# Performance work log

Hardware: AMD Instinct MI355X
Metric: run time of the kernel (lower is better)

## Reference

```python
import jax, jax.numpy as jnp
import numpy as np

B, C, H, W = 64, 3, 64, 64
F = 96          # base_filters
K = 8           # n_mixtures
h, w = H // 2, W // 2
C0 = 2 * C      # channels of each checkerboard half
SECTIONS = [C0, C0, C0 * K, C0 * K, C0 * K]
SPLITS = [int(s) for s in np.cumsum(SECTIONS)[:-1]]
EPS = 1e-6


def conv2d(x, wgt, b):
    y = jax.lax.conv_general_dilated(x, wgt, (1, 1), 'SAME',
                                     dimension_numbers=('NCHW', 'OIHW', 'NCHW'))
    return y + b[None, :, None, None]


def layer_norm(x, g, b, eps=1e-5):
    # nn.LayerNorm(mid_shape): normalize over (C,H,W) per sample
    mu = jnp.mean(x, axis=(1, 2, 3), keepdims=True)
    var = jnp.var(x, axis=(1, 2, 3), keepdims=True)
    return (x - mu) / jnp.sqrt(var + eps) * g[None] + b[None]


def checker_split(z, odd=False):
    Bz, Cz, Hz, Wz = z.shape
    z = z.reshape(Bz, Cz, Hz // 2, 2, Wz // 2, 2)
    p00 = z[:, :, :, 0, :, 0]; p01 = z[:, :, :, 0, :, 1]
    p10 = z[:, :, :, 1, :, 0]; p11 = z[:, :, :, 1, :, 1]
    z0 = jnp.concatenate([p00, p11], axis=1)  # even checkerboard
    z1 = jnp.concatenate([p01, p10], axis=1)  # odd checkerboard
    if odd:
        z0, z1 = z1, z0
    return z0, z1


def checker_merge(z0, z1, odd=False):
    if odd:
        z0, z1 = z1, z0
    Cz = z0.shape[1] // 2
    p00, p11 = z0[:, :Cz], z0[:, Cz:]
    p01, p10 = z1[:, :Cz], z1[:, Cz:]
    Bz, _, hz, wz = p00.shape
    zi = jnp.stack([jnp.stack([p00, p01], axis=-1),
                    jnp.stack([p10, p11], axis=-1)], axis=-2)  # (B,C,h,w,2i,2j)
    z = zi.transpose(0, 1, 2, 4, 3, 5).reshape(Bz, Cz, 2 * hz, 2 * wz)
    return z


def gated_attn(x, qkv_w, qkv_b, proj_w, proj_b):
    Bx, Fx, hx, wx = x.shape
    xf = x.reshape(Bx, Fx, hx * wx).transpose(0, 2, 1)  # (B, L, F)
    qkv = xf @ qkv_w.T + qkv_b
    q, k, v = jnp.split(qkv, 3, axis=-1)
    scores = jnp.einsum('bqf,bkf->bqk', q, k) / jnp.sqrt(jnp.float32(Fx))
    attn = jax.nn.softmax(scores, axis=-1)
    o = jnp.einsum('bqk,bkf->bqf', attn, v)
    g = o @ proj_w.T + proj_b
    ga, gb = jnp.split(g, 2, axis=-1)
    out = xf + ga * jax.nn.sigmoid(gb)  # gated residual
    return out.transpose(0, 2, 1).reshape(Bx, Fx, hx, wx)


def conditioner(z1, conv1_w, conv1_b, gconv_w, gconv_b, ln1_g, ln1_b,
                qkv_w, qkv_b, proj_w, proj_b, ln2_g, ln2_b, conv2_w, conv2_b):
    x = conv2d(z1, conv1_w, conv1_b)
    g = conv2d(x, gconv_w, gconv_b)
    ga, gb = jnp.split(g, 2, axis=1)
    x = x + ga * jax.nn.sigmoid(gb)          # GatedConv2d
    x = layer_norm(x, ln1_g, ln1_b)
    x = gated_attn(x, qkv_w, qkv_b, proj_w, proj_b)
    x = layer_norm(x, ln2_g, ln2_b)
    return conv2d(x, conv2_w, conv2_b)


def _forward(z, log_df_dz, conv1_w, conv1_b, gconv_w, gconv_b, ln1_g, ln1_b,
             qkv_w, qkv_b, proj_w, proj_b, ln2_g, ln2_b, conv2_w, conv2_b,
             a_log_scale, a_bias):
    z0, z1 = checker_split(z)
    params = conditioner(z1, conv1_w, conv1_b, gconv_w, gconv_b, ln1_g, ln1_b,
                         qkv_w, qkv_b, proj_w, proj_b, ln2_g, ln2_b, conv2_w, conv2_b)
    a, b, logpi, mu, s = jnp.split(params, SPLITS, axis=1)
    a = jnp.tanh(a) * a_log_scale + a_bias
    Bz = z0.shape[0]
    logpi = jax.nn.log_softmax(logpi.reshape(Bz, K, C0, h, w), axis=1)
    mu = mu.reshape(Bz, K, C0, h, w)
    s = s.reshape(Bz, K, C0, h, w)
    # mixture-of-logistics CDF
    u = (z0[:, None] - mu) * jnp.exp(-s)
    x = jnp.sum(jnp.exp(logpi) * jax.nn.sigmoid(u), axis=1)
    log_pdf = jax.scipy.special.logsumexp(
        logpi - s + jax.nn.log_sigmoid(u) + jax.nn.log_sigmoid(-u), axis=1)
    log_df_dz = log_df_dz + jnp.sum(log_pdf.reshape(Bz, -1), axis=1)
    # logit transform
    x = jnp.clip(x, EPS, 1.0 - EPS)
    z0n = jnp.log(x) - jnp.log1p(-x)
    log_df_dz = log_df_dz + jnp.sum((-jnp.log(x) - jnp.log1p(-x)).reshape(Bz, -1), axis=1)
    # affine rescale
    z0n = z0n * jnp.exp(a) + b
    log_df_dz = log_df_dz + jnp.sum(a.reshape(Bz, -1), axis=1)
    return checker_merge(z0n, z1), log_df_dz


def setup_inputs() -> dict:
    key = jax.random.key(0)
    ks = jax.random.split(key, 10)
    sc = 0.05
    return dict(
        z=jax.random.normal(ks[0], (B, C, H, W), jnp.float32),
        log_df_dz=jnp.zeros((B,), jnp.float32),
        conv1_w=sc * jax.random.normal(ks[1], (F, C0, 3, 3), jnp.float32),
        conv1_b=jnp.zeros((F,), jnp.float32),
        gconv_w=sc * jax.random.normal(ks[2], (2 * F, F, 3, 3), jnp.float32),
        gconv_b=jnp.zeros((2 * F,), jnp.float32),
        ln1_g=jnp.ones((F, h, w), jnp.float32),
        ln1_b=jnp.zeros((F, h, w), jnp.float32),
        qkv_w=sc * jax.random.normal(ks[3], (3 * F, F), jnp.float32),
        qkv_b=jnp.zeros((3 * F,), jnp.float32),
        proj_w=sc * jax.random.normal(ks[4], (2 * F, F), jnp.float32),
        proj_b=jnp.zeros((2 * F,), jnp.float32),
        ln2_g=jnp.ones((F, h, w), jnp.float32),
        ln2_b=jnp.zeros((F, h, w), jnp.float32),
        conv2_w=sc * jax.random.normal(ks[5], (sum(SECTIONS), F, 3, 3), jnp.float32),
        conv2_b=jnp.zeros((sum(SECTIONS),), jnp.float32),
        a_log_scale=0.01 * jax.random.normal(ks[6], (1,), jnp.float32),
        a_bias=0.01 * jax.random.normal(ks[7], (1,), jnp.float32),
    )


def reference(z, log_df_dz, conv1_w, conv1_b, gconv_w, gconv_b, ln1_g, ln1_b,
              qkv_w, qkv_b, proj_w, proj_b, ln2_g, ln2_b, conv2_w, conv2_b,
              a_log_scale, a_bias):
    return _forward(z, log_df_dz, conv1_w, conv1_b, gconv_w, gconv_b, ln1_g, ln1_b,
                    qkv_w, qkv_b, proj_w, proj_b, ln2_g, ln2_b, conv2_w, conv2_b,
                    a_log_scale, a_bias)
```

## Files before the change

kernel.cpp:

```cpp
#include <hip/hip_runtime.h>
#include <cstdint>
#include <cstddef>


typedef unsigned short u16;
typedef __attribute__((ext_vector_type(8))) short short8;
typedef __attribute__((ext_vector_type(4))) float f32x4;
typedef __attribute__((ext_vector_type(16))) float f32x16;

__device__ __forceinline__ float sigm(float x){ return 1.0f/(1.0f+__expf(-x)); }

__device__ __forceinline__ u16 f2bf(float f){
    unsigned int u = __float_as_uint(f);
    u += 0x7fffu + ((u >> 16) & 1u);
    return (u16)(u >> 16);
}
__device__ __forceinline__ float bf2f(u16 v){
    unsigned int u = ((unsigned int)v) << 16;
    return __uint_as_float(u);
}

__global__ __launch_bounds__(256) void k_prep(
    const float* __restrict__ z, const float* __restrict__ c1w, const float* __restrict__ c1b,
    const float* __restrict__ gw, const float* __restrict__ c2w,
    const float* __restrict__ qkvw, const float* __restrict__ pw,
    const float* __restrict__ ln1g, const float* __restrict__ ln1b,
    const float* __restrict__ ln2g, const float* __restrict__ ln2b,
    const float* __restrict__ logdf,
    u16* __restrict__ x1b,
    u16* __restrict__ Wg, u16* __restrict__ W2,
    u16* __restrict__ Wqkv, u16* __restrict__ Wproj,
    float* __restrict__ gt1, float* __restrict__ bt1,
    float* __restrict__ gt2, float* __restrict__ bt2,
    float* __restrict__ outlog)
{
    int blk = blockIdx.x;
    int tid = threadIdx.x;
    __shared__ float tin[6][6][34];
    __shared__ __align__(16) u16 Wc[96][72];
    __shared__ __align__(16) u16 imc[128][72];

    if (blk < 512){
        int b  = blk >> 3;
        int pg = blk & 7;
        int r0 = pg*4;
        for (int e = tid; e < 96*72; e += 256){
            int oc = e/72, k = e%72;
            Wc[oc][k] = (k < 54) ? f2bf(c1w[oc*54 + k]) : (u16)0;
        }
        for (int idx = tid; idx < 6*6*34; idx += 256){
            int c = idx/204, rem = idx%204;
            int rr = rem/34, q = rem%34;
            int ii = r0 - 1 + rr, jj = q - 1;
            float v = 0.f;
            if ((unsigned)ii < 32u && (unsigned)jj < 32u){
                if (c < 3) v = z[((b*3+c)*64 + 2*ii)*64 + (2*jj+1)];
                else       v = z[((b*3+(c-3))*64 + (2*ii+1))*64 + 2*jj];
            }
            tin[c][rr][q] = v;
        }
        __syncthreads();
        for (int e = tid; e < 128*72; e += 256){
            int px = e/72, k = e%72;
            float v = 0.f;
            if (k < 54){
                int c = k/9, rr = (k%9)/3, dcc = k%3;
                v = tin[c][(px>>5)+rr][(px&31)+dcc];
            }
            imc[px][k] = f2bf(v);
        }
        __syncthreads();

        int w = tid >> 6, lane = tid & 63;
        int cc = lane & 15, gg = lane >> 4;
        f32x4 acc[2][6];
        #pragma unroll
        for (int u=0;u<2;++u)
            #pragma unroll
            for (int t=0;t<6;++t) acc[u][t] = (f32x4){0.f,0.f,0.f,0.f};

        #pragma unroll
        for (int ks=0; ks<2; ++ks){
            short8 a0 = *reinterpret_cast<const short8*>(&imc[w*32 + cc     ][ks*32 + 8*gg]);
            short8 a1 = *reinterpret_cast<const short8*>(&imc[w*32 + 16 + cc][ks*32 + 8*gg]);
            #pragma unroll
            for (int t=0; t<6; ++t){
                short8 bb = *reinterpret_cast<const short8*>(&Wc[t*16+cc][ks*32 + 8*gg]);
                acc[0][t] = __builtin_amdgcn_mfma_f32_16x16x32_bf16(a0, bb, acc[0][t], 0,0,0);
                acc[1][t] = __builtin_amdgcn_mfma_f32_16x16x32_bf16(a1, bb, acc[1][t], 0,0,0);
            }
        }

        #pragma unroll
        for (int u=0;u<2;++u){
            int p0 = pg*128 + w*32 + u*16 + gg*4;
            #pragma unroll
            for (int t=0;t<6;++t){
                int oc = t*16+cc;
                float bv = c1b[oc];
                #pragma unroll
                for (int r=0;r<4;++r)
                    x1b[((size_t)(b*1024) + p0 + r)*96 + oc] = f2bf(acc[u][t][r] + bv);
            }
        }
    } else if (blk < 1160){
        int idx = (blk-512)*256 + tid;
        int tap = idx / (192*96);
        int rem = idx - tap*192*96;
        int ocp = rem / 96, ic = rem % 96;
        int obk = ocp/96, r = ocp%96, isB = r/48, i = r%48;
        int oc = obk*48 + i + isB*96;
        Wg[idx] = f2bf(gw[(size_t)(oc*96+ic)*9 + tap]);
    } else if (blk < 1700){
        int idx = (blk-1160)*256 + tid;
        int tap = idx / (160*96);
        int rem = idx - tap*160*96;
        int oc = rem / 96, ic = rem % 96;
        W2[idx] = (oc < 156) ? f2bf(c2w[(size_t)(oc*96+ic)*9 + tap]) : (u16)0;
    } else if (blk < 1808){
        int idx = (blk-1700)*256 + tid;
        Wqkv[idx] = f2bf(qkvw[idx]);
    } else if (blk < 1880){
        int idx = (blk-1808)*256 + tid;
        int ocp = idx / 96, ic = idx % 96;
        int obk = ocp/96, r = ocp%96, isB = r/48, i = r%48;
        int oc = obk*48 + i + isB*96;
        Wproj[idx] = f2bf(pw[(size_t)oc*96 + ic]);
    } else if (blk < 2264){
        int idx = (blk-1880)*256 + tid;
        int c = idx >> 10, p = idx & 1023;
        gt1[p*96 + c] = ln1g[idx];
    } else if (blk < 2648){
        int idx = (blk-2264)*256 + tid;
        int c = idx >> 10, p = idx & 1023;
        bt1[p*96 + c] = ln1b[idx];
    } else if (blk < 3032){
        int idx = (blk-2648)*256 + tid;
        int c = idx >> 10, p = idx & 1023;
        gt2[p*96 + c] = ln2g[idx];
    } else if (blk < 3416){
        int idx = (blk-3032)*256 + tid;
        int c = idx >> 10, p = idx & 1023;
        bt2[p*96 + c] = ln2b[idx];
    } else {
        if (tid < 64) outlog[tid] = logdf[tid];
    }
}

__global__ __launch_bounds__(256,4) void k_gconv(const u16* __restrict__ Xpb,
    const u16* __restrict__ Wt, const float* __restrict__ bias,
    u16* __restrict__ outb, float* __restrict__ partials)
{
    int blk  = blockIdx.x;
    int obk  = blk & 1;
    int pblk = (blk >> 1) & 7;
    int b    = blk >> 4;
    int tid  = threadIdx.x;
    int w = tid >> 6, lane = tid & 63;
    int cc = lane & 15, gg = lane >> 4;

    __shared__ __align__(16) u16 Ws[96][104];
    __shared__ float red[8];

    f32x4 acc[2][6];
    #pragma unroll
    for (int u=0;u<2;++u)
        #pragma unroll
        for (int t=0;t<6;++t) acc[u][t] = (f32x4){0.f,0.f,0.f,0.f};

    int base = pblk*128 + w*32;
    int ia = base >> 5;
    const u16* xb = Xpb + (size_t)b*1024*96;
    const u16* wbase = Wt + (size_t)obk*96*96;

    short8 wreg[5];
    #pragma unroll
    for (int i=0;i<5;++i){
        int c = tid + 256*i;
        if (c < 1152){
            int oc=c/12, ico=(c%12)*8;
            wreg[i] = *reinterpret_cast<const short8*>(wbase + oc*96 + ico);
        }
    }

    for (int tap=0; tap<9; ++tap){
        int dr = tap/3 - 1, dc = tap%3 - 1;
        __syncthreads();
        #pragma unroll
        for (int i=0;i<5;++i){
            int c = tid + 256*i;
            if (c < 1152){
                int oc=c/12, ico=(c%12)*8;
                *reinterpret_cast<short8*>(&Ws[oc][ico]) = wreg[i];
            }
        }
        if (tap < 8){
            const u16* wn = wbase + (size_t)(tap+1)*192*96;
            #pragma unroll
            for (int i=0;i<5;++i){
                int c = tid + 256*i;
                if (c < 1152){
                    int oc=c/12, ico=(c%12)*8;
                    wreg[i] = *reinterpret_cast<const short8*>(wn + oc*96 + ico);
                }
            }
        }
        __syncthreads();

        int ii = ia + dr;
        int jj0 = cc + dc, jj1 = cc + 16 + dc;
        bool rv = ((unsigned)ii < 32u);
        bool v0 = rv && ((unsigned)jj0 < 32u);
        bool v1 = rv && ((unsigned)jj1 < 32u);
        const u16* ar0 = xb + (ptrdiff_t)(ii*32 + jj0)*96 + 8*gg;
        const u16* ar1 = xb + (ptrdiff_t)(ii*32 + jj1)*96 + 8*gg;

        #pragma unroll
        for (int ks=0; ks<3; ++ks){
            short8 a0 = {0,0,0,0,0,0,0,0};
            short8 a1 = {0,0,0,0,0,0,0,0};
            if (v0) a0 = *reinterpret_cast<const short8*>(ar0 + ks*32);
            if (v1) a1 = *reinterpret_cast<const short8*>(ar1 + ks*32);
            #pragma unroll
            for (int t=0; t<6; ++t){
                short8 bb = *reinterpret_cast<const short8*>(&Ws[t*16+cc][ks*32+8*gg]);
                acc[0][t] = __builtin_amdgcn_mfma_f32_16x16x32_bf16(a0, bb, acc[0][t], 0,0,0);
                acc[1][t] = __builtin_amdgcn_mfma_f32_16x16x32_bf16(a1, bb, acc[1][t], 0,0,0);
            }
        }
    }

    float s = 0.f, ssq = 0.f;
    #pragma unroll
    for (int u=0;u<2;++u){
        int p0 = base + u*16 + gg*4;
        #pragma unroll
        for (int t=0;t<3;++t){
            int ocA = obk*48 + t*16+cc;
            float ba = bias[ocA], bbv = bias[ocA+96];
            #pragma unroll
            for (int r=0;r<4;++r){
                float res = bf2f(Xpb[((size_t)b*1024 + p0+r)*96 + ocA]);
                float va = acc[u][t][r]   + ba;
                float vb = acc[u][t+3][r] + bbv;
                float v = res + va*sigm(vb);
                outb[((size_t)b*1024 + p0+r)*96 + ocA] = f2bf(v);
                s += v; ssq += v*v;
            }
        }
    }
    #pragma unroll
    for (int o=32;o>0;o>>=1){ s += __shfl_down(s,o,64); ssq += __shfl_down(ssq,o,64); }
    if (lane==0){ red[w]=s; red[4+w]=ssq; }
    __syncthreads();
    if (tid==0){
        int slot = b*16 + pblk*2 + obk;
        partials[slot*2+0] = red[0]+red[1]+red[2]+red[3];
        partials[slot*2+1] = red[4]+red[5]+red[6]+red[7];
    }
}

__global__ __launch_bounds__(256) void k_lne(const u16* __restrict__ xb,
    const float* __restrict__ gt, const float* __restrict__ bt,
    const float* __restrict__ partials, u16* __restrict__ out)
{
    int b = blockIdx.x / 48, rem = blockIdx.x % 48;
    float s=0.f, ss=0.f;
    #pragma unroll
    for (int i=0;i<16;++i){ s += partials[(b*16+i)*2]; ss += partials[(b*16+i)*2+1]; }
    float mu = s/98304.f;
    float r = rsqrtf(ss/98304.f - mu*mu + 1e-5f);

    int e8 = rem*256 + threadIdx.x;
    size_t base = (size_t)b*98304 + (size_t)e8*8;
    short8 x8 = *reinterpret_cast<const short8*>(xb + base);
    const float* gp = gt + e8*8;
    const float* bp = bt + e8*8;
    short8 o8;
    #pragma unroll
    for (int i=0;i<8;++i)
        o8[i] = (short)f2bf((bf2f((u16)x8[i]) - mu)*r*gp[i] + bp[i]);
    *reinterpret_cast<short8*>(out + base) = o8;
}

__global__ __launch_bounds__(256,4) void k_conv2m(const u16* __restrict__ Xpb,
    const u16* __restrict__ Wt, const float* __restrict__ bias,
    u16* __restrict__ out)
{
    int blk  = blockIdx.x;
    int obk  = blk & 1;
    int pblk = (blk >> 1) & 7;
    int b    = blk >> 4;
    int tid  = threadIdx.x;
    int w = tid >> 6, lane = tid & 63;
    int cc = lane & 15, gg = lane >> 4;

    __shared__ __align__(16) u16 Ws[80][104];

    f32x4 acc[2][5];
    #pragma unroll
    for (int u=0;u<2;++u)
        #pragma unroll
        for (int t=0;t<5;++t) acc[u][t] = (f32x4){0.f,0.f,0.f,0.f};

    int base = pblk*128 + w*32;
    int ia = base >> 5;
    const u16* xb = Xpb + (size_t)b*1024*96;
    const u16* wbase = Wt + (size_t)obk*80*96;

    short8 wreg[4];
    #pragma unroll
    for (int i=0;i<4;++i){
        int c = tid + 256*i;
        if (c < 960){
            int oc=c/12, ico=(c%12)*8;
            wreg[i] = *reinterpret_cast<const short8*>(wbase + oc*96 + ico);
        }
    }

    for (int tap=0; tap<9; ++tap){
        int dr = tap/3 - 1, dc = tap%3 - 1;
        __syncthreads();
        #pragma unroll
        for (int i=0;i<4;++i){
            int c = tid + 256*i;
            if (c < 960){
                int oc=c/12, ico=(c%12)*8;
                *reinterpret_cast<short8*>(&Ws[oc][ico]) = wreg[i];
            }
        }
        if (tap < 8){
            const u16* wn = wbase + (size_t)(tap+1)*160*96;
            #pragma unroll
            for (int i=0;i<4;++i){
                int c = tid + 256*i;
                if (c < 960){
                    int oc=c/12, ico=(c%12)*8;
                    wreg[i] = *reinterpret_cast<const short8*>(wn + oc*96 + ico);
                }
            }
        }
        __syncthreads();

        int ii = ia + dr;
        int jj0 = cc + dc, jj1 = cc + 16 + dc;
        bool rv = ((unsigned)ii < 32u);
        bool v0 = rv && ((unsigned)jj0 < 32u);
        bool v1 = rv && ((unsigned)jj1 < 32u);
        const u16* ar0 = xb + (ptrdiff_t)(ii*32 + jj0)*96 + 8*gg;
        const u16* ar1 = xb + (ptrdiff_t)(ii*32 + jj1)*96 + 8*gg;

        #pragma unroll
        for (int ks=0; ks<3; ++ks){
            short8 a0 = {0,0,0,0,0,0,0,0};
            short8 a1 = {0,0,0,0,0,0,0,0};
            if (v0) a0 = *reinterpret_cast<const short8*>(ar0 + ks*32);
            if (v1) a1 = *reinterpret_cast<const short8*>(ar1 + ks*32);
            #pragma unroll
            for (int t=0; t<5; ++t){
                short8 bb = *reinterpret_cast<const short8*>(&Ws[t*16+cc][ks*32+8*gg]);
                acc[0][t] = __builtin_amdgcn_mfma_f32_16x16x32_bf16(a0, bb, acc[0][t], 0,0,0);
                acc[1][t] = __builtin_amdgcn_mfma_f32_16x16x32_bf16(a1, bb, acc[1][t], 0,0,0);
            }
        }
    }

    #pragma unroll
    for (int u=0;u<2;++u){
        int p0 = base + u*16 + gg*4;
        #pragma unroll
        for (int t=0;t<5;++t){
            int oc = obk*80 + t*16+cc;
            if (oc < 156){
                float bv = bias[oc];
                u16* op = out + ((size_t)b*156 + oc)*1024 + p0;
                #pragma unroll
                for (int r=0;r<4;++r) op[r] = f2bf(acc[u][t][r] + bv);
            }
        }
    }
}

__global__ __launch_bounds__(256,4) void k_qkvm(const u16* __restrict__ Xpb,
    const u16* __restrict__ Wt, const float* __restrict__ bias,
    u16* __restrict__ Qb, u16* __restrict__ Kf, u16* __restrict__ Vf)
{
    int blk  = blockIdx.x;
    int obk  = blk & 1;
    int pblk = (blk >> 1) & 7;
    int b    = blk >> 4;
    int tid  = threadIdx.x;
    int w = tid >> 6, lane = tid & 63;
    int cc = lane & 15, gg = lane >> 4;
    const float scale = 0.10206207262f;

    __shared__ __align__(16) u16 Ws[144][104];
    {
        const u16* wp = Wt + (size_t)obk*144*96;
        for (int c = tid; c < 144*12; c += 256){
            int oc = c/12, ico = (c%12)*8;
            *reinterpret_cast<short8*>(&Ws[oc][ico]) =
                *reinterpret_cast<const short8*>(wp + oc*96 + ico);
        }
    }

    f32x4 acc[2][9];
    #pragma unroll
    for (int u=0;u<2;++u)
        #pragma unroll
        for (int t=0;t<9;++t) acc[u][t] = (f32x4){0.f,0.f,0.f,0.f};

    int base = pblk*128 + w*32;
    const u16* xb = Xpb + ((size_t)b*1024 + base)*96;
    __syncthreads();

    #pragma unroll
    for (int ks=0; ks<3; ++ks){
        short8 a0 = *reinterpret_cast<const short8*>(xb + (size_t)cc*96      + ks*32 + 8*gg);
        short8 a1 = *reinterpret_cast<const short8*>(xb + (size_t)(cc+16)*96 + ks*32 + 8*gg);
        #pragma unroll
        for (int t=0; t<9; ++t){
            short8 bb = *reinterpret_cast<const short8*>(&Ws[t*16+cc][ks*32+8*gg]);
            acc[0][t] = __builtin_amdgcn_mfma_f32_16x16x32_bf16(a0, bb, acc[0][t], 0,0,0);
            acc[1][t] = __builtin_amdgcn_mfma_f32_16x16x32_bf16(a1, bb, acc[1][t], 0,0,0);
        }
    }

    #pragma unroll
    for (int u=0;u<2;++u){
        int p0 = base + u*16 + gg*4;
        #pragma unroll
        for (int t=0;t<9;++t){
            int n = obk*144 + t*16+cc;
            float bv = bias[n];
            #pragma unroll
            for (int r=0;r<4;++r){
                int p = p0 + r;
                float av = acc[u][t][r] + bv;
                if (n < 96){
                    Qb[((size_t)(b*1024+p))*96 + n] = f2bf(av*scale);
                } else if (n < 192){
                    int f = n-96;
                    int jt = p>>6, kl = p&63;
                    int tt = kl>>5;
                    int lanep = (kl&31) + 32*((f>>3)&1);
                    int ks = f>>4, j = f&7;
                    Kf[(size_t)(b*16+jt)*6144 + (size_t)(((tt*6+ks)*64 + lanep))*8 + j] = f2bf(av);
                } else {
                    int f = n-192;
                    int jt = p>>6, kl = p&63;
                    int ks2 = kl>>4, hi = (kl>>3)&1, j = kl&7;
                    int ft2 = f>>5;
                    int lanep = (f&31) + 32*hi;
                    Vf[(size_t)(b*16+jt)*6144 + (size_t)(((ft2*4+ks2)*64 + lanep))*8 + j] = f2bf(av);
                }
            }
        }
    }
}

__global__ __launch_bounds__(128,2) void k_attn(const u16* __restrict__ Qb,
    const u16* __restrict__ Kf, const u16* __restrict__ Vf, u16* __restrict__ Ob)
{
    int qt = blockIdx.x >> 6;
    int b  = blockIdx.x & 63;
    int tid = threadIdx.x;
    int w  = tid >> 6;
    int lane = tid & 63;
    int ln32 = lane & 31;
    int hl = lane >> 5;

    __shared__ __align__(16) u16 Ks[6144];
    __shared__ __align__(16) u16 Vs[6144];
    __shared__ __align__(16) u16 Ps[2][2112];

    int q0 = qt*64 + w*32;

    short8 qf[6];
    {
        const u16* qrow = Qb + ((size_t)(b*1024 + q0 + ln32))*96 + hl*8;
        #pragma unroll
        for (int ks=0; ks<6; ++ks)
            qf[ks] = *reinterpret_cast<const short8*>(qrow + ks*16);
    }

    f32x16 Oacc[3];
    #pragma unroll
    for (int ft=0; ft<3; ++ft)
        #pragma unroll
        for (int r=0; r<16; ++r) Oacc[ft][r] = 0.f;
    float l_acc[16];
    #pragma unroll
    for (int r=0; r<16; ++r) l_acc[r] = 0.f;

    const u16* Kb0 = Kf + (size_t)(b*16)*6144;
    const u16* Vb0 = Vf + (size_t)(b*16)*6144;

    short8 kreg[6], vreg[6];
    #pragma unroll
    for (int i=0;i<6;++i){
        int s8 = (tid + 128*i)*8;
        kreg[i] = *reinterpret_cast<const short8*>(Kb0 + s8);
        vreg[i] = *reinterpret_cast<const short8*>(Vb0 + s8);
    }

    for (int jt=0; jt<16; ++jt){
        __syncthreads();
        #pragma unroll
        for (int i=0;i<6;++i){
            int s8 = (tid + 128*i)*8;
            *reinterpret_cast<short8*>(Ks + s8) = kreg[i];
            *reinterpret_cast<short8*>(Vs + s8) = vreg[i];
        }
        if (jt < 15){
            const u16* kn = Kb0 + (size_t)(jt+1)*6144;
            const u16* vn = Vb0 + (size_t)(jt+1)*6144;
            #pragma unroll
            for (int i=0;i<6;++i){
                int s8 = (tid + 128*i)*8;
                kreg[i] = *reinterpret_cast<const short8*>(kn + s8);
                vreg[i] = *reinterpret_cast<const short8*>(vn + s8);
            }
        }
        __syncthreads();

        f32x16 Sacc[2];
        #pragma unroll
        for (int t=0;t<2;++t)
            #pragma unroll
            for (int r=0;r<16;++r) Sacc[t][r] = 0.f;
        #pragma unroll
        for (int ks=0; ks<6; ++ks){
            #pragma unroll
            for (int t=0; t<2; ++t){
                short8 bb = *reinterpret_cast<const short8*>(Ks + ((t*6+ks)*64 + lane)*8);
                Sacc[t] = __builtin_amdgcn_mfma_f32_32x32x16_bf16(qf[ks], bb, Sacc[t], 0,0,0);
            }
        }

        #pragma unroll
        for (int t=0; t<2; ++t){
            int off0 = (t*2 + (ln32>>4))*528 + ((ln32>>3)&1)*264 + (lane&7);
            #pragma unroll
            for (int r=0; r<16; ++r){
                int q = 4*hl + (r&3) + 8*(r>>2);
                float p = __expf(Sacc[t][r]);
                l_acc[r] += p;
                Ps[w][off0 + q*8] = f2bf(p);
            }
        }

        #pragma unroll
        for (int ks2=0; ks2<4; ++ks2){
            short8 pa = *reinterpret_cast<const short8*>(&Ps[w][ks2*528 + hl*264 + ln32*8]);
            #pragma unroll
            for (int ft=0; ft<3; ++ft){
                short8 vb = *reinterpret_cast<const short8*>(Vs + ((ft*4+ks2)*64 + lane)*8);
                Oacc[ft] = __builtin_amdgcn_mfma_f32_32x32x16_bf16(pa, vb, Oacc[ft], 0,0,0);
            }
        }
    }

    #pragma unroll
    for (int r=0; r<16; ++r){
        #pragma unroll
        for (int msk=1; msk<32; msk<<=1)
            l_acc[r] += __shfl_xor(l_acc[r], msk, 64);
    }
    #pragma unroll
    for (int r=0; r<16; ++r){
        int q = 4*hl + (r&3) + 8*(r>>2);
        float linv = 1.0f / l_acc[r];
        #pragma unroll
        for (int ft=0; ft<3; ++ft)
            Ob[((size_t)(b*1024 + q0 + q))*96 + ft*32 + ln32] = f2bf(Oacc[ft][r]*linv);
    }
}

__global__ __launch_bounds__(256,4) void k_projm(const u16* __restrict__ Opb,
    const u16* __restrict__ Wt, const float* __restrict__ bias,
    const u16* __restrict__ xlnb, u16* __restrict__ outb, float* __restrict__ partials)
{
    int blk  = blockIdx.x;
    int obk  = blk & 1;
    int pblk = (blk >> 1) & 7;
    int b    = blk >> 4;
    int tid  = threadIdx.x;
    int w = tid >> 6, lane = tid & 63;
    int cc = lane & 15, gg = lane >> 4;

    __shared__ __align__(16) u16 Ws[96][104];
    __shared__ float red[8];
    {
        const u16* wp = Wt + (size_t)obk*96*96;
        for (int c = tid; c < 96*12; c += 256){
            int oc = c/12, ico = (c%12)*8;
            *reinterpret_cast<short8*>(&Ws[oc][ico]) =
                *reinterpret_cast<const short8*>(wp + oc*96 + ico);
        }
    }

    f32x4 acc[2][6];
    #pragma unroll
    for (int u=0;u<2;++u)
        #pragma unroll
        for (int t=0;t<6;++t) acc[u][t] = (f32x4){0.f,0.f,0.f,0.f};

    int base = pblk*128 + w*32;
    const u16* xb = Opb + ((size_t)b*1024 + base)*96;
    __syncthreads();

    #pragma unroll
    for (int ks=0; ks<3; ++ks){
        short8 a0 = *reinterpret_cast<const short8*>(xb + (size_t)cc*96      + ks*32 + 8*gg);
        short8 a1 = *reinterpret_cast<const short8*>(xb + (size_t)(cc+16)*96 + ks*32 + 8*gg);
        #pragma unroll
        for (int t=0; t<6; ++t){
            short8 bb = *reinterpret_cast<const short8*>(&Ws[t*16+cc][ks*32+8*gg]);
            acc[0][t] = __builtin_amdgcn_mfma_f32_16x16x32_bf16(a0, bb, acc[0][t], 0,0,0);
            acc[1][t] = __builtin_amdgcn_mfma_f32_16x16x32_bf16(a1, bb, acc[1][t], 0,0,0);
        }
    }

    const u16* resb = xlnb + (size_t)b*1024*96;
    float s = 0.f, ssq = 0.f;
    #pragma unroll
    for (int u=0;u<2;++u){
        int p0 = base + u*16 + gg*4;
        #pragma unroll
        for (int t=0;t<3;++t){
            int ocA = obk*48 + t*16+cc;
            float ba = bias[ocA], bbv = bias[ocA+96];
            #pragma unroll
            for (int r=0;r<4;++r){
                float ga = acc[u][t][r]   + ba;
                float gb = acc[u][t+3][r] + bbv;
                float res = bf2f(resb[(size_t)(p0+r)*96 + ocA]);
                float v = res + ga * sigm(gb);
                outb[((size_t)b*1024 + p0+r)*96 + ocA] = f2bf(v);
                s += v; ssq += v*v;
            }
        }
    }
    #pragma unroll
    for (int o=32;o>0;o>>=1){ s += __shfl_down(s,o,64); ssq += __shfl_down(ssq,o,64); }
    if (lane==0){ red[w]=s; red[4+w]=ssq; }
    __syncthreads();
    if (tid==0){
        int slot = b*16 + pblk*2 + obk;
        partials[slot*2+0] = red[0]+red[1]+red[2]+red[3];
        partials[slot*2+1] = red[4]+red[5]+red[6]+red[7];
    }
}

__global__ __launch_bounds__(256) void k_mix(const float* __restrict__ z,
    const u16* __restrict__ params, const float* __restrict__ a_ls_p,
    const float* __restrict__ a_b_p, float* __restrict__ out_z, float* __restrict__ out_log)
{
    int b = blockIdx.x / 24;
    int rem = blockIdx.x % 24;
    int c0 = rem / 4;
    int pix = (rem & 3)*256 + threadIdx.x;
    int i = pix >> 5, j = pix & 31;
    float als = a_ls_p[0], abv = a_b_p[0];
    const u16* pb = params + (size_t)b*156*1024;
    float logacc = 0.f;

    if (c0 < 3){
        int idx01 = ((b*3+c0)*64 + 2*i)*64 + 2*j+1;
        int idx10 = ((b*3+c0)*64 + 2*i+1)*64 + 2*j;
        out_z[idx01] = z[idx01];
        out_z[idx10] = z[idx10];
    }

    {
        float z0v = (c0<3) ? z[((b*3+c0)*64 + 2*i)*64 + 2*j]
                           : z[((b*3+(c0-3))*64 + 2*i+1)*64 + 2*j+1];
        float a_raw = bf2f(pb[(c0)*1024 + pix]);
        float bco   = bf2f(pb[(6+c0)*1024 + pix]);
        float lp[8], mu[8], sv[8];
        float m1 = -1e30f;
        #pragma unroll
        for (int k=0;k<8;++k){
            lp[k] = bf2f(pb[(12 + k*6 + c0)*1024 + pix]);
            mu[k] = bf2f(pb[(60 + k*6 + c0)*1024 + pix]);
            sv[k] = bf2f(pb[(108 + k*6 + c0)*1024 + pix]);
            m1 = fmaxf(m1, lp[k]);
        }
        float se = 0.f;
        #pragma unroll
        for (int k=0;k<8;++k) se += __expf(lp[k]-m1);
        float lse = m1 + __logf(se);
        float xm = 0.f, mt = -1e30f;
        float t[8];
        #pragma unroll
        for (int k=0;k<8;++k){
            float lpn = lp[k] - lse;
            float u = (z0v - mu[k]) * __expf(-sv[k]);
            float au = fabsf(u);
            xm += __expf(lpn) * (1.f/(1.f+__expf(-u)));
            float lss = -(au + 2.f*log1pf(__expf(-au)));
            float tk = lpn - sv[k] + lss;
            t[k] = tk; mt = fmaxf(mt, tk);
        }
        float se2 = 0.f;
        #pragma unroll
        for (int k=0;k<8;++k) se2 += __expf(t[k]-mt);
        logacc += mt + __logf(se2);
        xm = fminf(fmaxf(xm, 1e-6f), 1.f-1e-6f);
        float lx = __logf(xm), l1x = log1pf(-xm);
        logacc += -lx - l1x;
        float aa = tanhf(a_raw)*als + abv;
        float z0n = (lx - l1x)*__expf(aa) + bco;
        logacc += aa;
        int oidx = (c0<3) ? ((b*3+c0)*64 + 2*i)*64 + 2*j
                          : ((b*3+(c0-3))*64 + 2*i+1)*64 + 2*j+1;
        out_z[oidx] = z0n;
    }

    #pragma unroll
    for (int o=32;o>0;o>>=1) logacc += __shfl_down(logacc, o, 64);
    __shared__ float part[4];
    if ((threadIdx.x&63)==0) part[threadIdx.x>>6] = logacc;
    __syncthreads();
    if (threadIdx.x==0){
        atomicAdd(out_log + b, part[0]+part[1]+part[2]+part[3]);
    }
}

extern "C" void kernel_launch(void* const* d_in, const int* in_sizes, int n_in,
                              void* d_out, int out_size, void* d_ws, size_t ws_size,
                              hipStream_t stream)
{
    const float* z     = (const float*)d_in[0];
    const float* logdf = (const float*)d_in[1];
    const float* c1w   = (const float*)d_in[2];
    const float* c1b   = (const float*)d_in[3];
    const float* gw    = (const float*)d_in[4];
    const float* gcb   = (const float*)d_in[5];
    const float* ln1g  = (const float*)d_in[6];
    const float* ln1b  = (const float*)d_in[7];
    const float* qkvw  = (const float*)d_in[8];
    const float* qkvb  = (const float*)d_in[9];
    const float* pw    = (const float*)d_in[10];
    const float* pbb   = (const float*)d_in[11];
    const float* ln2g  = (const float*)d_in[12];
    const float* ln2b  = (const float*)d_in[13];
    const float* c2w   = (const float*)d_in[14];
    const float* c2b   = (const float*)d_in[15];
    const float* als   = (const float*)d_in[16];
    const float* ab    = (const float*)d_in[17];

    float* out_z   = (float*)d_out;
    float* out_log = out_z + 786432;

    float* ws     = (float*)d_ws;
    u16*   x1b    = (u16*)(ws + 0);
    u16*   xg_b   = (u16*)(ws + 3145728);
    u16*   xlnb   = (u16*)(ws + 6291456);
    u16*   Vf     = (u16*)(ws + 9437184);
    u16*   Ob     = (u16*)(ws + 12582912);
    u16*   x2b    = (u16*)(ws + 15728640);
    u16*   Qb     = x1b;
    u16*   Kf     = xg_b;
    u16*   xln2b  = xlnb;
    u16*   params = (u16*)(ws + 9437184);
    const size_t T = 19660800;
    float* gt1    = ws + T;
    float* bt1    = ws + T + 98304;
    float* gt2    = ws + T + 196608;
    float* bt2    = ws + T + 294912;
    float* part1  = ws + T + 393216;
    float* part2  = ws + T + 395264;
    u16*   Wg     = (u16*)(ws + T + 397568);
    u16*   W2     = (u16*)(ws + T + 480512);
    u16*   Wqkv   = (u16*)(ws + T + 549632);
    u16*   Wproj  = (u16*)(ws + T + 563456);

    k_prep   <<<3417, 256, 0, stream>>>(z, c1w, c1b, gw, c2w, qkvw, pw,
                                        ln1g, ln1b, ln2g, ln2b, logdf,
                                        x1b, Wg, W2, Wqkv, Wproj,
                                        gt1, bt1, gt2, bt2, out_log);
    k_gconv  <<<1024, 256, 0, stream>>>(x1b, Wg, gcb, xg_b, part1);
    k_lne    <<<3072, 256, 0, stream>>>(xg_b, gt1, bt1, part1, xlnb);
    k_qkvm   <<<1024, 256, 0, stream>>>(xlnb, Wqkv, qkvb, Qb, Kf, Vf);
    k_attn   <<<1024, 128, 0, stream>>>(Qb, Kf, Vf, Ob);
    k_projm  <<<1024, 256, 0, stream>>>(Ob, Wproj, pbb, xlnb, x2b, part2);
    k_lne    <<<3072, 256, 0, stream>>>(x2b, gt2, bt2, part2, xln2b);
    k_conv2m <<<1024, 256, 0, stream>>>(xln2b, W2, c2b, params);
    k_mix    <<<1536, 256, 0, stream>>>(z, params, als, ab, out_z, out_log);
}
```

Before: 290.2 us.

## Split attention keys across waves and read K/V directly from global memory

Each 128-thread attention block now covers 32 queries instead of 64, and the grid doubles. The two waves each process half of the 16 key tiles for the same queries. Partial outputs and row sums are combined through a padded LDS buffer, and one wave writes the normalized result. The shared-memory K/V staging with its per-tile barriers is removed in favor of direct global (cache) reads, with occupancy hints raised to 3 blocks. This trades LDS reuse across waves for more parallelism and fewer syncs, at the cost of duplicated K/V cache traffic and a final cross-wave reduction.

```diff
diff --git a/kernel.cpp b/kernel.cpp
--- a/kernel.cpp
+++ b/kernel.cpp
@@ -459,7 +459,7 @@
     }
 }
 
-__global__ __launch_bounds__(128,2) void k_attn(const u16* __restrict__ Qb,
+__global__ __launch_bounds__(128,3) void k_attn(const u16* __restrict__ Qb,
     const u16* __restrict__ Kf, const u16* __restrict__ Vf, u16* __restrict__ Ob)
 {
     int qt = blockIdx.x >> 6;
@@ -470,11 +470,10 @@
     int ln32 = lane & 31;
     int hl = lane >> 5;
 
-    __shared__ __align__(16) u16 Ks[6144];
-    __shared__ __align__(16) u16 Vs[6144];
     __shared__ __align__(16) u16 Ps[2][2112];
-
-    int q0 = qt*64 + w*32;
+    __shared__ float Cmb[64][65];
+
+    int q0 = qt*32;
 
     short8 qf[6];
     {
@@ -496,33 +495,9 @@
     const u16* Kb0 = Kf + (size_t)(b*16)*6144;
     const u16* Vb0 = Vf + (size_t)(b*16)*6144;
 
-    short8 kreg[6], vreg[6];
-    #pragma unroll
-    for (int i=0;i<6;++i){
-        int s8 = (tid + 128*i)*8;
-        kreg[i] = *reinterpret_cast<const short8*>(Kb0 + s8);
-        vreg[i] = *reinterpret_cast<const short8*>(Vb0 + s8);
-    }
-
-    for (int jt=0; jt<16; ++jt){
-        __syncthreads();
-        #pragma unroll
-        for (int i=0;i<6;++i){
-            int s8 = (tid + 128*i)*8;
-            *reinterpret_cast<short8*>(Ks + s8) = kreg[i];
-            *reinterpret_cast<short8*>(Vs + s8) = vreg[i];
-        }
-        if (jt < 15){
-            const u16* kn = Kb0 + (size_t)(jt+1)*6144;
-            const u16* vn = Vb0 + (size_t)(jt+1)*6144;
-            #pragma unroll
-            for (int i=0;i<6;++i){
-                int s8 = (tid + 128*i)*8;
-                kreg[i] = *reinterpret_cast<const short8*>(kn + s8);
-                vreg[i] = *reinterpret_cast<const short8*>(vn + s8);
-            }
-        }
-        __syncthreads();
+    for (int jt = w*8; jt < w*8 + 8; ++jt){
+        const u16* kt = Kb0 + (size_t)jt*6144;
+        const u16* vt = Vb0 + (size_t)jt*6144;
 
         f32x16 Sacc[2];
         #pragma unroll
@@ -533,7 +508,7 @@
         for (int ks=0; ks<6; ++ks){
             #pragma unroll
             for (int t=0; t<2; ++t){
-                short8 bb = *reinterpret_cast<const short8*>(Ks + ((t*6+ks)*64 + lane)*8);
+                short8 bb = *reinterpret_cast<const short8*>(kt + ((t*6+ks)*64 + lane)*8);
                 Sacc[t] = __builtin_amdgcn_mfma_f32_32x32x16_bf16(qf[ks], bb, Sacc[t], 0,0,0);
             }
         }
@@ -555,7 +530,7 @@
             short8 pa = *reinterpret_cast<const short8*>(&Ps[w][ks2*528 + hl*264 + ln32*8]);
             #pragma unroll
             for (int ft=0; ft<3; ++ft){
-                short8 vb = *reinterpret_cast<const short8*>(Vs + ((ft*4+ks2)*64 + lane)*8);
+                short8 vb = *reinterpret_cast<const short8*>(vt + ((ft*4+ks2)*64 + lane)*8);
                 Oacc[ft] = __builtin_amdgcn_mfma_f32_32x32x16_bf16(pa, vb, Oacc[ft], 0,0,0);
             }
         }
@@ -567,13 +542,28 @@
         for (int msk=1; msk<32; msk<<=1)
             l_acc[r] += __shfl_xor(l_acc[r], msk, 64);
     }
-    #pragma unroll
-    for (int r=0; r<16; ++r){
-        int q = 4*hl + (r&3) + 8*(r>>2);
-        float linv = 1.0f / l_acc[r];
+
+    if (w == 1){
         #pragma unroll
         for (int ft=0; ft<3; ++ft)
-            Ob[((size_t)(b*1024 + q0 + q))*96 + ft*32 + ln32] = f2bf(Oacc[ft][r]*linv);
+            #pragma unroll
+            for (int r=0; r<16; ++r) Cmb[lane][ft*16+r] = Oacc[ft][r];
+        #pragma unroll
+        for (int r=0; r<16; ++r) Cmb[lane][48+r] = l_acc[r];
+    }
+    __syncthreads();
+    if (w == 0){
+        #pragma unroll
+        for (int r=0; r<16; ++r){
+            float lt = l_acc[r] + Cmb[lane][48+r];
+            float linv = 1.0f / lt;
+            int q = 4*hl + (r&3) + 8*(r>>2);
+            #pragma unroll
+            for (int ft=0; ft<3; ++ft){
+                float o = Oacc[ft][r] + Cmb[lane][ft*16+r];
+                Ob[((size_t)(b*1024 + q0 + q))*96 + ft*32 + ln32] = f2bf(o*linv);
+            }
+        }
     }
 }
 
@@ -784,7 +774,7 @@
     k_gconv  <<<1024, 256, 0, stream>>>(x1b, Wg, gcb, xg_b, part1);
     k_lne    <<<3072, 256, 0, stream>>>(xg_b, gt1, bt1, part1, xlnb);
     k_qkvm   <<<1024, 256, 0, stream>>>(xlnb, Wqkv, qkvb, Qb, Kf, Vf);
-    k_attn   <<<1024, 128, 0, stream>>>(Qb, Kf, Vf, Ob);
+    k_attn   <<<2048, 128, 0, stream>>>(Qb, Kf, Vf, Ob);
     k_projm  <<<1024, 256, 0, stream>>>(Ob, Wproj, pbb, xlnb, x2b, part2);
     k_lne    <<<3072, 256, 0, stream>>>(x2b, gt2, bt2, part2, xln2b);
     k_conv2m <<<1024, 256, 0, stream>>>(xln2b, W2, c2b, params);
```

After: 347.1 us. 19.6% more time.
